# Kernel tuning notes

Hardware: AMD Instinct MI355X
Metric: run time of the kernel (lower is better)

The kernel has to match this reference:

```python
import jax, jax.numpy as jnp
import numpy as np

N = 8192      # collocation points
H = 128       # hidden width of the stream-function MLP


def setup_inputs() -> dict:
    key = jax.random.key(0)
    ks = jax.random.split(key, 9)
    s = lambda fan_in: 1.0 / np.sqrt(fan_in)
    return {
        "x":  jax.random.normal(ks[0], (N, 3), dtype=jnp.float32),
        "W1": jax.random.normal(ks[1], (3, H), dtype=jnp.float32) * s(3),
        "b1": jnp.zeros((H,), dtype=jnp.float32),
        "W2": jax.random.normal(ks[2], (H, H), dtype=jnp.float32) * s(H),
        "b2": jnp.zeros((H,), dtype=jnp.float32),
        "W3": jax.random.normal(ks[3], (H, H), dtype=jnp.float32) * s(H),
        "b3": jnp.zeros((H,), dtype=jnp.float32),
        "W4": jax.random.normal(ks[4], (H, 1), dtype=jnp.float32) * s(H),
        "b4": jnp.zeros((1,), dtype=jnp.float32),
        "nu": jnp.float32(1.0),
    }


def reference(x, W1, b1, W2, b2, W3, b3, W4, b4, nu):
    # psi: scalar stream function of a single sample xi = (x, y, t)
    def psi(xi):
        h = jnp.tanh(xi @ W1 + b1)
        h = jnp.tanh(h @ W2 + b2)
        h = jnp.tanh(h @ W3 + b3)
        return (h @ W4 + b4)[0]

    # vorticity w = dv/dx - du/dy = -(psi_xx + psi_yy)
    def w_fn(xi):
        Hpsi = jax.hessian(psi)(xi)          # [3,3]
        return -(Hpsi[0, 0] + Hpsi[1, 1])

    def per_sample(xi):
        g = jax.grad(psi)(xi)                # dpsi: [3]
        u = g[1]
        v = -g[0]
        dw = jax.grad(w_fn)(xi)              # [dwdx, dwdy, dwdt]
        Hw = jax.hessian(w_fn)(xi)           # 4th-order derivs of psi
        lapw = Hw[0, 0] + Hw[1, 1]
        nse = dw[2] + dw[0] * u + dw[1] * v - nu * lapw
        return jnp.stack([u, v]), nse

    f, NSE = jax.vmap(per_sample)(x)         # f: [N,2], NSE: [N]
    return f, NSE
```

## Files before the change

kernel.cpp:

```cpp
#include <hip/hip_runtime.h>
#include <hip/hip_bf16.h>

#define NSAMP 8192
#define HD 128
#define NC 18
#define SB 8
#define NCOLS 144
#define KSTR 136

typedef __attribute__((ext_vector_type(8))) short bf16x8;
typedef __attribute__((ext_vector_type(4))) float f32x4;
typedef float f2 __attribute__((ext_vector_type(2)));


__device__ __forceinline__ unsigned packf2(f2 v) {
    __hip_bfloat162 h = __float22bfloat162_rn(float2{v.x, v.y});
    return *(unsigned*)&h;
}
__device__ __forceinline__ f2 unpk(unsigned r) {
    f2 v;
    v.x = __uint_as_float(r << 16);
    v.y = __uint_as_float(r & 0xffff0000u);
    return v;
}

__device__ __forceinline__ void tanh_jet2(const f2* __restrict__ f,
                                          f2* __restrict__ out) {
    f2 y;  y.x = tanhf(f[0].x);  y.y = tanhf(f[0].y);
    const f2 one = {1.0f, 1.0f};
    const f2 s  = one - y*y;
    const f2 t2 = -y*s;
    const f2 t3 = s*(y*y - 0.3333333333333333f);
    const f2 t4 = y*s*(one + one - 3.0f*y*y) * 0.3333333333333333f;
    const f2 tp1 = f[1]+f[1], tp2 = f[2]+f[2], tp3 = f[3]+f[3], tp4 = f[4]+f[4];
    f2 P[18];
    P[4]  = f[1]*f[1];
    P[5]  = tp1*f[2];
    P[6]  = f[2]*f[2];
    P[7]  = tp1*f[3];
    P[8]  = tp2*f[3];
    P[9]  = tp1*f[4];
    P[10] = tp1*f[5]  + tp2*f[4];
    P[11] = tp1*f[6]  + tp2*f[5];
    P[12] = tp2*f[6];
    P[13] = tp1*f[7]  + tp3*f[4];
    P[14] = tp2*f[8]  + tp3*f[6];
    P[15] = tp1*f[9]  + f[4]*f[4];
    P[16] = tp1*f[11] + tp2*f[10] + tp4*f[6] + f[5]*f[5];
    P[17] = tp2*f[12] + f[6]*f[6];
    f2 q[18];
    q[0] = t2;
    q[1] = t3*f[1];  q[2] = t3*f[2];  q[3] = t3*f[3];
#pragma unroll
    for (int m = 4; m <= 17; ++m) q[m] = t3*f[m] + t4*P[m];
    out[0] = y;
    out[1] = s*f[1];  out[2] = s*f[2];  out[3] = s*f[3];
    out[4] = s*f[4]  + P[4]*q[0];
    out[5] = s*f[5]  + P[5]*q[0];
    out[6] = s*f[6]  + P[6]*q[0];
    out[7] = s*f[7]  + P[7]*q[0];
    out[8] = s*f[8]  + P[8]*q[0];
    out[9]  = s*f[9]  + P[9]*q[0]  + P[4]*q[1];
    out[10] = s*f[10] + P[10]*q[0] + P[5]*q[1] + P[4]*q[2];
    out[11] = s*f[11] + P[11]*q[0] + P[6]*q[1] + P[5]*q[2];
    out[12] = s*f[12] + P[12]*q[0] + P[6]*q[2];
    out[13] = s*f[13] + P[13]*q[0] + P[7]*q[1] + P[4]*q[3];
    out[14] = s*f[14] + P[14]*q[0] + P[8]*q[2] + P[6]*q[3];
    out[15] = s*f[15] + P[15]*q[0] + P[9]*q[1] + P[4]*q[4];
    out[16] = s*f[16] + P[16]*q[0] + P[11]*q[1] + P[10]*q[2]
            + P[4]*q[6] + P[6]*q[4] + P[5]*q[5];
    out[17] = s*f[17] + P[17]*q[0] + P[12]*q[2] + P[6]*q[6];
}

__device__ __forceinline__ void tanh_jet_lin2(f2 f0, f2 p1, f2 p2, f2 p3,
                                              f2* __restrict__ out) {
    f2 y;  y.x = tanhf(f0.x);  y.y = tanhf(f0.y);
    const f2 one = {1.0f, 1.0f};
    const f2 s  = one - y*y;
    const f2 t2 = -y*s;
    const f2 t3 = s*(y*y - 0.3333333333333333f);
    const f2 t4 = y*s*(one + one - 3.0f*y*y) * 0.3333333333333333f;
    const f2 tp1 = p1+p1, tp2 = p2+p2;
    const f2 P4 = p1*p1, P5 = tp1*p2, P6 = p2*p2, P7 = tp1*p3, P8 = tp2*p3;
    const f2 q0 = t2;
    const f2 q1 = t3*p1, q2 = t3*p2, q3 = t3*p3;
    const f2 q4 = t4*P4, q5 = t4*P5, q6 = t4*P6;
    out[0] = y;
    out[1] = s*p1;  out[2] = s*p2;  out[3] = s*p3;
    out[4] = P4*q0; out[5] = P5*q0; out[6] = P6*q0;
    out[7] = P7*q0; out[8] = P8*q0;
    out[9]  = P4*q1;
    out[10] = P4*q2 + P5*q1;
    out[11] = P5*q2 + P6*q1;
    out[12] = P6*q2;
    out[13] = P4*q3 + P7*q1;
    out[14] = P6*q3 + P8*q2;
    out[15] = P4*q4;
    out[16] = P4*q6 + P6*q4 + P5*q5;
    out[17] = P6*q6;
}

__global__ __launch_bounds__(256)
void transpose_w(const float* __restrict__ W2, const float* __restrict__ W3,
                 unsigned* __restrict__ wsT) {
    const int id = blockIdx.x * 256 + threadIdx.x;
    if (id >= 2 * HD * (HD / 2)) return;
    const int L  = id / (HD * (HD / 2));
    const int r  = id % (HD * (HD / 2));
    const int j  = r / (HD / 2);
    const int kp = r % (HD / 2);
    const float* W = L ? W3 : W2;
    wsT[id] = packf2(f2{W[(2 * kp) * HD + j], W[(2 * kp + 1) * HD + j]});
}

__global__ __launch_bounds__(512, 4)
void hydro_main(const float* __restrict__ x,
                const float* __restrict__ W1, const float* __restrict__ b1,
                const float* __restrict__ b2, const float* __restrict__ b3,
                const float* __restrict__ W4, const float* __restrict__ nu_p,
                const unsigned short* __restrict__ wsT,
                float* __restrict__ out) {
    __shared__ __align__(16) unsigned short Hl[NCOLS * KSTR];
    __shared__ float psis[NCOLS];

    const int tid = threadIdx.x;
    const int wv  = tid >> 6;
    const int ln  = tid & 63;
    const int s0  = blockIdx.x * SB;
    const int s   = tid >> 6;
    const int jp  = tid & 63;

    {
        const float xs = x[3 * (s0 + s) + 0];
        const float ys = x[3 * (s0 + s) + 1];
        const float ts = x[3 * (s0 + s) + 2];
        const int j0 = 2 * jp;
        const f2 wx = *(const f2*)&W1[j0];
        const f2 wy = *(const f2*)&W1[HD + j0];
        const f2 wt = *(const f2*)&W1[2 * HD + j0];
        const f2 bb = *(const f2*)&b1[j0];
        f2 h[NC];
        const f2 fc = wx * xs + wy * ys + wt * ts + bb;
        tanh_jet_lin2(fc, wx, wy, wt, h);
#pragma unroll
        for (int c = 0; c < NC; ++c)
            *(unsigned*)&Hl[(s * NC + c) * KSTR + j0] = packf2(h[c]);
    }
    __syncthreads();

    const int lr   = ln & 15;
    const int koff = (ln >> 4) * 8;

#pragma unroll 1
    for (int L = 0; L < 2; ++L) {
        const unsigned short* __restrict__ WT = wsT + L * HD * HD;
        bf16x8 Af[4];
#pragma unroll
        for (int ks = 0; ks < 4; ++ks)
            Af[ks] = *(const bf16x8*)&WT[(wv * 16 + lr) * HD + ks * 32 + koff];
        f32x4 acc[9];
#pragma unroll
        for (int nt = 0; nt < 9; ++nt) acc[nt] = (f32x4)0.0f;
#pragma unroll
        for (int ks = 0; ks < 4; ++ks) {
#pragma unroll
            for (int nt = 0; nt < 9; ++nt) {
                const bf16x8 Bf = *(const bf16x8*)&Hl[(nt * 16 + lr) * KSTR + ks * 32 + koff];
                acc[nt] = __builtin_amdgcn_mfma_f32_16x16x32_bf16(Af[ks], Bf, acc[nt], 0, 0, 0);
            }
        }
        __syncthreads();
#pragma unroll
        for (int nt = 0; nt < 9; ++nt) {
            const int n = nt * 16 + lr;
            const int m = wv * 16 + (ln >> 4) * 4;
            uint2 w;
            w.x = packf2(f2{acc[nt].x, acc[nt].y});
            w.y = packf2(f2{acc[nt].z, acc[nt].w});
            *(uint2*)&Hl[n * KSTR + m] = w;
        }
        __syncthreads();
        {
            const float* bL = L ? b3 : b2;
            const int j0 = 2 * jp;
            f2 fa[NC], ha[NC];
#pragma unroll
            for (int c = 0; c < NC; ++c)
                fa[c] = unpk(*(const unsigned*)&Hl[(s * NC + c) * KSTR + j0]);
            fa[0] += *(const f2*)&bL[j0];
            tanh_jet2(fa, ha);
#pragma unroll
            for (int c = 0; c < NC; ++c)
                *(unsigned*)&Hl[(s * NC + c) * KSTR + j0] = packf2(ha[c]);
        }
        __syncthreads();
    }

    if (tid < NCOLS) {
        float acc = 0.0f;
#pragma unroll
        for (int kk = 0; kk < 16; ++kk) {
            const uint4 q = *(const uint4*)&Hl[tid * KSTR + kk * 8];
            const int k = kk * 8;
            const f2 e0 = unpk(q.x), e1 = unpk(q.y), e2 = unpk(q.z), e3 = unpk(q.w);
            acc = fmaf(e0.x, W4[k + 0], acc);
            acc = fmaf(e0.y, W4[k + 1], acc);
            acc = fmaf(e1.x, W4[k + 2], acc);
            acc = fmaf(e1.y, W4[k + 3], acc);
            acc = fmaf(e2.x, W4[k + 4], acc);
            acc = fmaf(e2.y, W4[k + 5], acc);
            acc = fmaf(e3.x, W4[k + 6], acc);
            acc = fmaf(e3.y, W4[k + 7], acc);
        }
        psis[tid] = acc;
    }
    __syncthreads();

    if (tid < SB) {
        const float* p = &psis[tid * NC];
        const float nu = nu_p[0];
        const float u  = p[2];
        const float v  = -p[1];
        const float wx = -(6.0f * p[9]  + 2.0f * p[11]);
        const float wy = -(2.0f * p[10] + 6.0f * p[12]);
        const float wt = -(2.0f * p[13] + 2.0f * p[14]);
        const float lapw = -(24.0f * p[15] + 8.0f * p[16] + 24.0f * p[17]);
        const float nse  = wt + wx * u + wy * v - nu * lapw;
        const int gi = s0 + tid;
        out[2 * gi]         = u;
        out[2 * gi + 1]     = v;
        out[2 * NSAMP + gi] = nse;
    }
}

extern "C" void kernel_launch(void* const* d_in, const int* in_sizes, int n_in,
                              void* d_out, int out_size, void* d_ws, size_t ws_size,
                              hipStream_t stream) {
    const float* x  = (const float*)d_in[0];
    const float* W1 = (const float*)d_in[1];
    const float* b1 = (const float*)d_in[2];
    const float* W2 = (const float*)d_in[3];
    const float* b2 = (const float*)d_in[4];
    const float* W3 = (const float*)d_in[5];
    const float* b3 = (const float*)d_in[6];
    const float* W4 = (const float*)d_in[7];
    const float* nu = (const float*)d_in[9];
    float* out = (float*)d_out;

    unsigned* wsT = (unsigned*)d_ws;
    hipLaunchKernelGGL(transpose_w, dim3(64), dim3(256), 0, stream, W2, W3, wsT);
    hipLaunchKernelGGL(hydro_main, dim3(NSAMP / SB), dim3(512), 0, stream,
                       x, W1, b1, b2, b3, W4, nu,
                       (const unsigned short*)d_ws, out);
}
```

Baseline: 97.37 us.

## Drop weight-transpose kernel, load W directly, use fast tanh, raise occupancy

Removes the separate transpose_w launch and has each wave gather its bf16 A-fragments straight from the fp32 W2/W3 in global memory with strided loads, converting on the fly. It replaces library tanhf with an exp/reciprocal formulation and raises the launch-bounds occupancy hint from 4 to 8. The aim is to save one kernel launch and cut transcendental cost. The trade-offs are uncoalesced strided weight loads repeated by every block, possible precision or overflow issues in the fast tanh for large inputs, and register pressure from the higher occupancy target.

```diff
diff --git a/kernel.cpp b/kernel.cpp
--- a/kernel.cpp
+++ b/kernel.cpp
@@ -24,9 +24,20 @@
     return v;
 }
 
+__device__ __forceinline__ f2 ftanh2(f2 v) {
+    const float ex = __expf(v.x * 2.0f);
+    const float ey = __expf(v.y * 2.0f);
+    const float rx = __builtin_amdgcn_rcpf(ex + 1.0f);
+    const float ry = __builtin_amdgcn_rcpf(ey + 1.0f);
+    f2 r;
+    r.x = 1.0f - (rx + rx);
+    r.y = 1.0f - (ry + ry);
+    return r;
+}
+
 __device__ __forceinline__ void tanh_jet2(const f2* __restrict__ f,
                                           f2* __restrict__ out) {
-    f2 y;  y.x = tanhf(f[0].x);  y.y = tanhf(f[0].y);
+    const f2 y = ftanh2(f[0]);
     const f2 one = {1.0f, 1.0f};
     const f2 s  = one - y*y;
     const f2 t2 = -y*s;
@@ -74,7 +85,7 @@
 
 __device__ __forceinline__ void tanh_jet_lin2(f2 f0, f2 p1, f2 p2, f2 p3,
                                               f2* __restrict__ out) {
-    f2 y;  y.x = tanhf(f0.x);  y.y = tanhf(f0.y);
+    const f2 y = ftanh2(f0);
     const f2 one = {1.0f, 1.0f};
     const f2 s  = one - y*y;
     const f2 t2 = -y*s;
@@ -100,25 +111,12 @@
     out[17] = P6*q6;
 }
 
-__global__ __launch_bounds__(256)
-void transpose_w(const float* __restrict__ W2, const float* __restrict__ W3,
-                 unsigned* __restrict__ wsT) {
-    const int id = blockIdx.x * 256 + threadIdx.x;
-    if (id >= 2 * HD * (HD / 2)) return;
-    const int L  = id / (HD * (HD / 2));
-    const int r  = id % (HD * (HD / 2));
-    const int j  = r / (HD / 2);
-    const int kp = r % (HD / 2);
-    const float* W = L ? W3 : W2;
-    wsT[id] = packf2(f2{W[(2 * kp) * HD + j], W[(2 * kp + 1) * HD + j]});
-}
-
-__global__ __launch_bounds__(512, 4)
+__global__ __launch_bounds__(512, 8)
 void hydro_main(const float* __restrict__ x,
                 const float* __restrict__ W1, const float* __restrict__ b1,
-                const float* __restrict__ b2, const float* __restrict__ b3,
+                const float* __restrict__ W2, const float* __restrict__ b2,
+                const float* __restrict__ W3, const float* __restrict__ b3,
                 const float* __restrict__ W4, const float* __restrict__ nu_p,
-                const unsigned short* __restrict__ wsT,
                 float* __restrict__ out) {
     __shared__ __align__(16) unsigned short Hl[NCOLS * KSTR];
     __shared__ float psis[NCOLS];
@@ -153,11 +151,18 @@
 
 #pragma unroll 1
     for (int L = 0; L < 2; ++L) {
-        const unsigned short* __restrict__ WT = wsT + L * HD * HD;
+        const float* __restrict__ Wg = L ? W3 : W2;
         bf16x8 Af[4];
 #pragma unroll
-        for (int ks = 0; ks < 4; ++ks)
-            Af[ks] = *(const bf16x8*)&WT[(wv * 16 + lr) * HD + ks * 32 + koff];
+        for (int ks = 0; ks < 4; ++ks) {
+            const float* wp = &Wg[(ks * 32 + koff) * HD + (wv * 16 + lr)];
+            const unsigned r0 = packf2(f2{wp[0 * HD], wp[1 * HD]});
+            const unsigned r1 = packf2(f2{wp[2 * HD], wp[3 * HD]});
+            const unsigned r2 = packf2(f2{wp[4 * HD], wp[5 * HD]});
+            const unsigned r3 = packf2(f2{wp[6 * HD], wp[7 * HD]});
+            const uint4 q{r0, r1, r2, r3};
+            Af[ks] = *(const bf16x8*)&q;
+        }
         f32x4 acc[9];
 #pragma unroll
         for (int nt = 0; nt < 9; ++nt) acc[nt] = (f32x4)0.0f;
@@ -247,9 +252,6 @@
     const float* nu = (const float*)d_in[9];
     float* out = (float*)d_out;
 
-    unsigned* wsT = (unsigned*)d_ws;
-    hipLaunchKernelGGL(transpose_w, dim3(64), dim3(256), 0, stream, W2, W3, wsT);
     hipLaunchKernelGGL(hydro_main, dim3(NSAMP / SB), dim3(512), 0, stream,
-                       x, W1, b1, b2, b3, W4, nu,
-                       (const unsigned short*)d_ws, out);
-}
+                       x, W1, b1, W2, b2, W3, b3, W4, nu, out);
+}
```

Measured after the change: 101.0 us. 1.04x slower.
